# Kernel optimization log

Measured on AMD Instinct MI355X. Metric: run time of the kernel, lower is better.

## Reference

```python
import jax, jax.numpy as jnp
import numpy as np

D_LATENT = 128
WIDTH = 64
MODES = 32
N_LAYERS = 4
N_INST = 8
LIFT_L = 64   # lift_shape = (width, 64)
B = 128
OUT_LEN = 4096
EPS = 1e-5


def _gelu(x):
    return jax.nn.gelu(x, approximate=False)  # torch nn.GELU default = exact erf


def setup_inputs() -> dict:
    key = jax.random.key(0)
    ks = jax.random.split(key, 16)
    n = lambda k, shape, s=0.02: (s * jax.random.normal(k, shape)).astype(jnp.float32)
    spec_scale = 1.0 / (WIDTH * WIDTH)
    return {
        "z": jax.random.normal(ks[0], (B, D_LATENT), dtype=jnp.float32),
        "instrument_params": jax.random.normal(ks[1], (B, N_INST), dtype=jnp.float32),
        "lift_w": n(ks[2], (D_LATENT, WIDTH * LIFT_L)),
        "lift_b": jnp.zeros((WIDTH * LIFT_L,), jnp.float32),
        "inst_w1": n(ks[3], (N_INST, WIDTH), 0.3),
        "inst_b1": jnp.zeros((WIDTH,), jnp.float32),
        "inst_w2": n(ks[4], (WIDTH, WIDTH), 0.1),
        "inst_b2": jnp.zeros((WIDTH,), jnp.float32),
        "spec_w": (spec_scale * jax.random.normal(ks[5], (N_LAYERS, WIDTH, WIDTH, MODES, 2))).astype(jnp.float32),
        "pw_w": n(ks[6], (N_LAYERS, WIDTH, WIDTH), 0.1),   # (layer, out, in)
        "pw_b": jnp.zeros((N_LAYERS, WIDTH), jnp.float32),
        "proj_w1": n(ks[7], (2 * WIDTH, WIDTH), 0.1),      # (out, in)
        "proj_b1": jnp.zeros((2 * WIDTH,), jnp.float32),
        "proj_w2": n(ks[8], (1, 2 * WIDTH), 0.1),
        "proj_b2": jnp.zeros((1,), jnp.float32),
        "out_len": OUT_LEN,
    }


def _interp_linear(x, out_len):
    # torch F.interpolate(mode='linear', align_corners=False)
    in_len = x.shape[-1]
    src = jnp.clip((jnp.arange(out_len, dtype=x.dtype) + 0.5) * (in_len / out_len) - 0.5, 0.0, in_len - 1)
    i0 = jnp.floor(src).astype(jnp.int32)
    i1 = jnp.minimum(i0 + 1, in_len - 1)
    w = src - i0.astype(x.dtype)
    return x[..., i0] * (1.0 - w) + x[..., i1] * w


def _spectral_conv(x, w):
    # x: (B, C, L) real; w: (C_in, C_out, modes, 2)
    L = x.shape[-1]
    xf = jnp.fft.rfft(x, axis=-1)                 # (B, C, L//2+1) complex64
    xr = jnp.real(xf[:, :, :MODES])
    xi = jnp.imag(xf[:, :, :MODES])
    wr, wi = w[..., 0], w[..., 1]
    out_r = jnp.einsum('bim,iom->bom', xr, wr) - jnp.einsum('bim,iom->bom', xi, wi)
    out_i = jnp.einsum('bim,iom->bom', xr, wi) + jnp.einsum('bim,iom->bom', xi, wr)
    n_freq = L // 2 + 1
    of = (out_r + 1j * out_i).astype(xf.dtype)
    of = jnp.pad(of, ((0, 0), (0, 0), (0, n_freq - MODES)))
    return jnp.fft.irfft(of, n=L, axis=-1)


def reference(z, instrument_params, lift_w, lift_b, inst_w1, inst_b1, inst_w2, inst_b2,
              spec_w, pw_w, pw_b, proj_w1, proj_b1, proj_w2, proj_b2, out_len):
    Bz = z.shape[0]
    x = (z @ lift_w + lift_b).reshape(Bz, WIDTH, LIFT_L)
    x = _interp_linear(x, out_len)                              # (B, W, L)
    cond = _gelu(instrument_params @ inst_w1 + inst_b1) @ inst_w2 + inst_b2
    x = x + cond[:, :, None]
    for l in range(N_LAYERS):
        x1 = _spectral_conv(x, spec_w[l])
        x2 = jnp.einsum('bil,oi->bol', x, pw_w[l]) + pw_b[l][None, :, None]
        h = x1 + x2
        mu = h.mean(axis=-1, keepdims=True)
        var = h.var(axis=-1, keepdims=True)                     # biased, like InstanceNorm1d
        x = _gelu((h - mu) * jax.lax.rsqrt(var + EPS))
    h = _gelu(jnp.einsum('bil,oi->bol', x, proj_w1) + proj_b1[None, :, None])
    out = jnp.einsum('bil,oi->bol', h, proj_w2) + proj_b2[None, :, None]
    return out[:, 0, :]                                         # (B, out_len)
```

## Files before the change

kernel.cpp:

```cpp
#include <hip/hip_runtime.h>
#include <math.h>


typedef _Float16 half8 __attribute__((ext_vector_type(8)));
typedef __attribute__((ext_vector_type(4))) float fx4;

__device__ __forceinline__ float gelu_f(float x){
    float u = x*x;
    float a = x * fmaf(-0.1029443f, u, -2.3022083f);
    float e = exp2f(a);
    float r = __builtin_amdgcn_rcpf(1.0f + e);
    return x * r;
}
__device__ __forceinline__ unsigned short f2h(float f){
    union { _Float16 h; unsigned short u; } c;
    c.h = (_Float16)f;
    return c.u;
}
__device__ __forceinline__ float h2f(unsigned short u){
    union { unsigned short u; _Float16 h; } c;
    c.u = u;
    return (float)c.h;
}

static const size_t OFF_XH    = 0;
static const size_t OFF_XT    = 16777216;
static const size_t OFF_TABB  = 33554432;
static const size_t OFF_TABT  = 33685504;
static const size_t OFF_MAH   = 33816576;
static const size_t OFF_PWWH  = 34078720;
static const size_t OFF_W1H   = 34086912;
static const size_t OFF_COND  = 34091008;
static const size_t OFF_STATS = 34099200;
static const size_t OFF_DFTP  = 34115584;
static const size_t OFF_X0    = 38309888;

__global__ void k_tab(unsigned short* __restrict__ tabB, unsigned short* __restrict__ tabT,
                      const float* __restrict__ pww, unsigned short* __restrict__ pwwh,
                      const float* __restrict__ pj1w, unsigned short* __restrict__ w1h){
    int t = blockIdx.x*256 + threadIdx.x;
    if (t < 16384) pwwh[t] = f2h(pww[t]);
    if (t < 8192)  w1h[t]  = f2h(pj1w[t]);
    int m2 = t >> 12, n = t & 4095;
    int m = m2 & 31;
    int r = (m*n) & 4095;
    int r2 = (r >= 2048) ? (r - 4096) : r;
    float a = (float)r2 * 1.5339807878856412e-3f;
    float v = (m2 >= 32) ? sinf(a) : cosf(a);
    tabB[(size_t)m2*4096 + n] = f2h(v);
    tabT[(size_t)n*64 + m2]   = f2h(v * 0.015625f);
}

__global__ __launch_bounds__(64) void k_cond(const float* __restrict__ instp,
        const float* __restrict__ w1, const float* __restrict__ b1,
        const float* __restrict__ w2, const float* __restrict__ b2,
        float* __restrict__ cond){
    int b = blockIdx.x, tid = threadIdx.x;
    __shared__ float ipl[8];
    __shared__ float tl[64];
    if (tid < 8) ipl[tid] = instp[b*8 + tid];
    __syncthreads();
    float s = b1[tid];
    #pragma unroll
    for (int k = 0; k < 8; ++k) s = fmaf(ipl[k], w1[k*64 + tid], s);
    tl[tid] = gelu_f(s);
    __syncthreads();
    float c = b2[tid];
    #pragma unroll 8
    for (int j = 0; j < 64; ++j) c = fmaf(tl[j], w2[j*64 + tid], c);
    cond[b*64 + tid] = c;
}

__global__ __launch_bounds__(256) void k_liftc(const float* __restrict__ z,
        const float* __restrict__ lw, const float* __restrict__ lb,
        const float* __restrict__ cond, float* __restrict__ x0){
    int b = blockIdx.x, q = blockIdx.y;
    int t = threadIdx.x;
    __shared__ float zl[128];
    if (t < 128) zl[t] = z[b*128 + t];
    __syncthreads();
    #pragma unroll
    for (int i = 0; i < 4; ++i){
        int e = q*1024 + i*256 + t;
        float s = lb[e];
        #pragma unroll 8
        for (int d = 0; d < 128; ++d)
            s = fmaf(zl[d], lw[(size_t)d*4096 + e], s);
        x0[(size_t)b*4096 + e] = s + cond[b*64 + (e >> 6)];
    }
}

template<int MODE, int DODFT>
__global__ __launch_bounds__(256) void k_prep(
        const unsigned short* __restrict__ xhp, const float* __restrict__ statsr,
        const unsigned short* __restrict__ tabB, const float* __restrict__ x0,
        unsigned short* __restrict__ xT, float* __restrict__ dftp)
{
    int b = blockIdx.x, ng = blockIdx.y;
    int t = threadIdx.x;
    int w = t >> 6, lane = t & 63;
    int lrow = lane & 15, g = lane >> 4;
    __shared__ __align__(16) unsigned short xl[2][4096];
    __shared__ float xs[(MODE == 2) ? 65*64 : 1];
    int co = t >> 2, nq = t & 3;
    float mu = 0.f, rs = 1.f;
    if (MODE == 1){
        float2 sr = *(const float2*)(statsr + (size_t)(b*64+co)*2);
        mu = sr.x * (1.f/4096.f);
        float var = fmaf(sr.y, 1.f/4096.f, -mu*mu);
        rs = rsqrtf(var + 1e-5f);
    }
    if (MODE == 2){
        const float* xb0 = x0 + (size_t)b*4096;
        #pragma unroll
        for (int i = 0; i < 16; ++i){
            int idx = i*256 + t;
            xs[(idx >> 6)*65 + (idx & 63)] = xb0[idx];
        }
        __syncthreads();
    }
    fx4 acc[4];
    #pragma unroll
    for (int i = 0; i < 4; ++i) acc[i] = (fx4){0.f,0.f,0.f,0.f};

    const unsigned short* hrow = xhp + ((size_t)(b*64+co))*4096 + ng*512 + nq*16;
    unsigned short* xtbase = xT + ((size_t)b*4096 + (size_t)ng*512)*64;

    uint4 cA, cB;
    if (MODE == 1){ cA = *(const uint4*)(hrow); cB = *(const uint4*)(hrow + 8); }
    for (int it = 0; it < 8; ++it){
        int n0 = ng*512 + it*64;
        char* xb = (char*)(&xl[it & 1][0]);
        uint4 nA, nB;
        if (MODE == 1 && it < 7){
            nA = *(const uint4*)(hrow + (it+1)*64);
            nB = *(const uint4*)(hrow + (it+1)*64 + 8);
        }
        unsigned int pk[8];
        if (MODE == 1){
            unsigned int hu[8] = {cA.x,cA.y,cA.z,cA.w,cB.x,cB.y,cB.z,cB.w};
            #pragma unroll
            for (int i = 0; i < 8; ++i){
                float f0 = h2f((unsigned short)(hu[i] & 0xFFFFu));
                float f1 = h2f((unsigned short)(hu[i] >> 16));
                f0 = gelu_f((f0 - mu)*rs);
                f1 = gelu_f((f1 - mu)*rs);
                pk[i] = (unsigned int)f2h(f0) | ((unsigned int)f2h(f1) << 16);
            }
        } else {
            const float* xr = xs + co*65;
            #pragma unroll
            for (int i = 0; i < 8; ++i){
                float v[2];
                #pragma unroll
                for (int q = 0; q < 2; ++q){
                    int n = n0 + nq*16 + i*2 + q;
                    float src = (n + 0.5f)*0.015625f - 0.5f;
                    src = fminf(fmaxf(src, 0.0f), 63.0f);
                    int i0 = (int)src;
                    int i1 = (i0 + 1 > 63) ? 63 : (i0 + 1);
                    float wt = src - (float)i0;
                    v[q] = xr[i0] + wt*(xr[i1] - xr[i0]);
                }
                pk[i] = (unsigned int)f2h(v[0]) | ((unsigned int)f2h(v[1]) << 16);
            }
        }
        unsigned int base = (unsigned int)co*128 + (unsigned int)nq*32;
        unsigned int sw = (unsigned int)((co & 7) << 4);
        *(uint4*)(xb + ((base +  0) ^ sw)) = make_uint4(pk[0],pk[1],pk[2],pk[3]);
        *(uint4*)(xb + ((base + 16) ^ sw)) = make_uint4(pk[4],pk[5],pk[6],pk[7]);
        __syncthreads();

        if (DODFT){
            int m0 = w*16;
            #pragma unroll
            for (int ks = 0; ks < 2; ++ks){
                int kk = ks*32 + g*8;
                half8 af = *(const half8*)(tabB + (size_t)(m0 + lrow)*4096 + n0 + kk);
                #pragma unroll
                for (int ct = 0; ct < 4; ++ct){
                    int row = ct*16 + lrow;
                    unsigned int ba = ((unsigned int)row*128 + (unsigned int)kk*2)
                                      ^ (unsigned int)((row & 7) << 4);
                    half8 bf = *(const half8*)(xb + ba);
                    acc[ct] = __builtin_amdgcn_mfma_f32_16x16x32_f16(af, bf, acc[ct], 0, 0, 0);
                }
            }
        }
        {
            int n = t & 63, coq = t >> 6;
            unsigned int opk[8];
            #pragma unroll
            for (int i = 0; i < 8; ++i){
                int r0 = coq*16 + 2*i, r1 = r0 + 1;
                unsigned int a0 = ((unsigned int)r0*128 + (unsigned int)n*2)
                                  ^ (unsigned int)((r0 & 7) << 4);
                unsigned int a1 = ((unsigned int)r1*128 + (unsigned int)n*2)
                                  ^ (unsigned int)((r1 & 7) << 4);
                unsigned short v0 = *(const unsigned short*)(xb + a0);
                unsigned short v1 = *(const unsigned short*)(xb + a1);
                opk[i] = (unsigned int)v0 | ((unsigned int)v1 << 16);
            }
            unsigned short* dst = xtbase + (size_t)(it*64 + n)*64 + coq*16;
            *(uint4*)dst       = make_uint4(opk[0],opk[1],opk[2],opk[3]);
            *(uint4*)(dst + 8) = make_uint4(opk[4],opk[5],opk[6],opk[7]);
        }
        if (MODE == 1 && it < 7){ cA = nA; cB = nB; }
    }
    if (DODFT){
        int m0 = w*16;
        #pragma unroll
        for (int ct = 0; ct < 4; ++ct){
            float4 v = make_float4(acc[ct][0], acc[ct][1], acc[ct][2], acc[ct][3]);
            *(float4*)(dftp + ((size_t)(b*8+ng)*64 + ct*16 + lrow)*64 + m0 + g*4) = v;
        }
    }
}

__global__ __launch_bounds__(256) void k_mix(const float* __restrict__ dftp,
        const float* __restrict__ specw, unsigned short* __restrict__ mah,
        float* __restrict__ statsr, int l){
    int b = blockIdx.x, coq = blockIdx.y, t = threadIdx.x;
    __shared__ float xm[64*64];
    if (t < 128) statsr[b*128 + t] = 0.f;
    const float* dp = dftp + (size_t)b*8*4096;
    #pragma unroll
    for (int i = 0; i < 4; ++i){
        int e = i*1024 + t*4;
        float4 s = make_float4(0.f,0.f,0.f,0.f);
        #pragma unroll
        for (int ng = 0; ng < 8; ++ng){
            float4 v = *(const float4*)(dp + (size_t)ng*4096 + e);
            s.x += v.x; s.y += v.y; s.z += v.z; s.w += v.w;
        }
        if (e & 32){ s.x = -s.x; s.y = -s.y; s.z = -s.z; s.w = -s.w; }
        *(float4*)(xm + e) = s;
    }
    __syncthreads();
    int mq = t & 3, ciq = (t >> 2) & 3, co_l = t >> 4;
    int co = coq*16 + co_l;
    float yr[8] = {0,0,0,0,0,0,0,0}, yi[8] = {0,0,0,0,0,0,0,0};
    const float* wbase = specw + (size_t)l*262144 + (size_t)co*64 + mq*16;
    #pragma unroll 4
    for (int cil = 0; cil < 16; ++cil){
        int ci = ciq*16 + cil;
        const float* wp = wbase + (size_t)ci*4096;
        float4 w0 = *(const float4*)(wp);
        float4 w1v = *(const float4*)(wp + 4);
        float4 w2v = *(const float4*)(wp + 8);
        float4 w3v = *(const float4*)(wp + 12);
        const float* xc = xm + ci*64 + mq*8;
        float4 r0 = *(const float4*)(xc);
        float4 r1 = *(const float4*)(xc + 4);
        float4 i0 = *(const float4*)(xc + 32);
        float4 i1 = *(const float4*)(xc + 36);
        float wr[8] = {w0.x,w0.z,w1v.x,w1v.z,w2v.x,w2v.z,w3v.x,w3v.z};
        float wi[8] = {w0.y,w0.w,w1v.y,w1v.w,w2v.y,w2v.w,w3v.y,w3v.w};
        float xr[8] = {r0.x,r0.y,r0.z,r0.w,r1.x,r1.y,r1.z,r1.w};
        float xi[8] = {i0.x,i0.y,i0.z,i0.w,i1.x,i1.y,i1.z,i1.w};
        #pragma unroll
        for (int mm = 0; mm < 8; ++mm){
            yr[mm] = fmaf(xr[mm], wr[mm], fmaf(-xi[mm], wi[mm], yr[mm]));
            yi[mm] = fmaf(xr[mm], wi[mm], fmaf( xi[mm], wr[mm], yi[mm]));
        }
    }
    #pragma unroll
    for (int mm = 0; mm < 8; ++mm){
        yr[mm] += __shfl_xor(yr[mm], 4); yr[mm] += __shfl_xor(yr[mm], 8);
        yi[mm] += __shfl_xor(yi[mm], 4); yi[mm] += __shfl_xor(yi[mm], 8);
    }
    if (ciq == 0){
        unsigned short* mb = mah + (size_t)(b*64 + co)*64;
        unsigned int pr[4], pi[4];
        #pragma unroll
        for (int p = 0; p < 4; ++p){
            int m0 = mq*8 + 2*p;
            float s0 = (m0 == 0) ? 0.015625f : 0.03125f;
            pr[p] = (unsigned int)f2h(s0*yr[2*p]) | ((unsigned int)f2h(0.03125f*yr[2*p+1]) << 16);
            pi[p] = (unsigned int)f2h(-0.03125f*yi[2*p]) | ((unsigned int)f2h(-0.03125f*yi[2*p+1]) << 16);
        }
        *(uint4*)(mb + mq*8)      = make_uint4(pr[0],pr[1],pr[2],pr[3]);
        *(uint4*)(mb + 32 + mq*8) = make_uint4(pi[0],pi[1],pi[2],pi[3]);
    }
}

__global__ __launch_bounds__(256, 4) void k_pass3(
        const unsigned short* __restrict__ xT, const unsigned short* __restrict__ tabT,
        const unsigned short* __restrict__ pwwh, const float* __restrict__ pwb,
        const unsigned short* __restrict__ mah, unsigned short* __restrict__ xh,
        float* __restrict__ statsr, int lay)
{
    int b = blockIdx.x, ntg = blockIdx.y;
    int t = threadIdx.x, w = t >> 6, lane = t & 63;
    int lrow = lane & 15, g = lane >> 4;
    int nsl = ntg*256 + w*64;

    half8 A[4][4];
    #pragma unroll
    for (int nt = 0; nt < 4; ++nt){
        int n = nsl + nt*16 + lrow;
        #pragma unroll
        for (int ks = 0; ks < 4; ++ks){
            int k = ks*32 + g*8;
            const unsigned short* src = (k < 64)
                ? (xT   + ((size_t)b*4096 + n)*64 + k)
                : (tabT + (size_t)n*64 + (k - 64));
            A[nt][ks] = *(const half8*)src;
        }
    }
    __shared__ float sred[2][4][64];
    #pragma unroll
    for (int cot = 0; cot < 4; ++cot){
        int co = cot*16 + lrow;
        half8 Bv[4];
        #pragma unroll
        for (int ks = 0; ks < 4; ++ks){
            int k = ks*32 + g*8;
            const unsigned short* src = (k < 64)
                ? (pwwh + ((size_t)lay*64 + co)*64 + k)
                : (mah  + ((size_t)b*64 + co)*64 + (k - 64));
            Bv[ks] = *(const half8*)src;
        }
        fx4 acc[4];
        #pragma unroll
        for (int i = 0; i < 4; ++i) acc[i] = (fx4){0.f,0.f,0.f,0.f};
        #pragma unroll
        for (int ks = 0; ks < 4; ++ks)
            #pragma unroll
            for (int nt = 0; nt < 4; ++nt)
                acc[nt] = __builtin_amdgcn_mfma_f32_16x16x32_f16(A[nt][ks], Bv[ks], acc[nt], 0, 0, 0);

        float pb = pwb[lay*64 + co];
        unsigned short* hr = xh + ((size_t)(b*64+co))*4096;
        float sS = 0.f, sQ = 0.f;
        #pragma unroll
        for (int nt = 0; nt < 4; ++nt){
            float h0 = acc[nt][0] + pb;
            float h1 = acc[nt][1] + pb;
            float h2 = acc[nt][2] + pb;
            float h3 = acc[nt][3] + pb;
            uint2 pk;
            pk.x = (unsigned int)f2h(h0) | ((unsigned int)f2h(h1) << 16);
            pk.y = (unsigned int)f2h(h2) | ((unsigned int)f2h(h3) << 16);
            *(uint2*)(hr + nsl + nt*16 + g*4) = pk;
            sS += (h0 + h1) + (h2 + h3);
            float q = h0*h0;
            q = fmaf(h1, h1, q); q = fmaf(h2, h2, q); q = fmaf(h3, h3, q);
            sQ += q;
        }
        sS += __shfl_xor(sS, 16); sQ += __shfl_xor(sQ, 16);
        sS += __shfl_xor(sS, 32); sQ += __shfl_xor(sQ, 32);
        if (g == 0){
            sred[0][w][cot*16 + lrow] = sS;
            sred[1][w][cot*16 + lrow] = sQ;
        }
    }
    __syncthreads();
    if (t < 64){
        float S = 0.f, Q = 0.f;
        #pragma unroll
        for (int ww = 0; ww < 4; ++ww){ S += sred[0][ww][t]; Q += sred[1][ww][t]; }
        atomicAdd(statsr + (size_t)(b*64+t)*2,     S);
        atomicAdd(statsr + (size_t)(b*64+t)*2 + 1, Q);
    }
}

__global__ __launch_bounds__(512) void k_proj(
        const unsigned short* __restrict__ xT, const unsigned short* __restrict__ w1h,
        const float* __restrict__ b1, const float* __restrict__ w2,
        const float* __restrict__ b2, float* __restrict__ out)
{
    int b = blockIdx.x, ntg = blockIdx.y;
    int t = threadIdx.x, w = t >> 6, lane = t & 63;
    int lrow = lane & 15, g = lane >> 4;
    int o2h = w & 1, nq = w >> 1;
    int nb = ntg*512 + nq*128;

    half8 A[4][2];
    #pragma unroll
    for (int ot = 0; ot < 4; ++ot)
        #pragma unroll
        for (int ks = 0; ks < 2; ++ks)
            A[ot][ks] = *(const half8*)(w1h + (size_t)(o2h*64 + ot*16 + lrow)*64 + ks*32 + g*8);
    float bb[16], wv[16];
    #pragma unroll
    for (int ot = 0; ot < 4; ++ot)
        #pragma unroll
        for (int j = 0; j < 4; ++j){
            int o2 = o2h*64 + ot*16 + g*4 + j;
            bb[ot*4+j] = b1[o2];
            wv[ot*4+j] = w2[o2];
        }
    __shared__ float sred[4][8][2][16];
    for (int tl = 0; tl < 8; ++tl){
        int n = nb + tl*16 + lrow;
        fx4 acc[4];
        #pragma unroll
        for (int i = 0; i < 4; ++i) acc[i] = (fx4){0.f,0.f,0.f,0.f};
        #pragma unroll
        for (int ks = 0; ks < 2; ++ks){
            half8 bf = *(const half8*)(xT + ((size_t)b*4096 + n)*64 + ks*32 + g*8);
            #pragma unroll
            for (int ot = 0; ot < 4; ++ot)
                acc[ot] = __builtin_amdgcn_mfma_f32_16x16x32_f16(A[ot][ks], bf, acc[ot], 0, 0, 0);
        }
        float p = 0.f;
        #pragma unroll
        for (int ot = 0; ot < 4; ++ot)
            #pragma unroll
            for (int j = 0; j < 4; ++j)
                p = fmaf(wv[ot*4+j], gelu_f(acc[ot][j] + bb[ot*4+j]), p);
        p += __shfl_xor(p, 16); p += __shfl_xor(p, 32);
        if (lane < 16) sred[nq][tl][o2h][lane] = p;
    }
    __syncthreads();
    {
        int cl = t & 15, tlf = (t >> 4) & 7, nqf = t >> 7;
        out[(size_t)b*4096 + ntg*512 + t] =
            sred[nqf][tlf][0][cl] + sred[nqf][tlf][1][cl] + b2[0];
    }
}

extern "C" void kernel_launch(void* const* d_in, const int* in_sizes, int n_in,
                              void* d_out, int out_size, void* d_ws, size_t ws_size,
                              hipStream_t stream) {
    (void)in_sizes; (void)n_in; (void)out_size; (void)ws_size;
    const float* z      = (const float*)d_in[0];
    const float* instp  = (const float*)d_in[1];
    const float* lift_w = (const float*)d_in[2];
    const float* lift_b = (const float*)d_in[3];
    const float* iw1    = (const float*)d_in[4];
    const float* ib1    = (const float*)d_in[5];
    const float* iw2    = (const float*)d_in[6];
    const float* ib2    = (const float*)d_in[7];
    const float* specw  = (const float*)d_in[8];
    const float* pww    = (const float*)d_in[9];
    const float* pwb    = (const float*)d_in[10];
    const float* pj1w   = (const float*)d_in[11];
    const float* pj1b   = (const float*)d_in[12];
    const float* pj2w   = (const float*)d_in[13];
    const float* pj2b   = (const float*)d_in[14];

    float* ws = (float*)d_ws;
    unsigned short* xh    = (unsigned short*)(ws + OFF_XH);
    unsigned short* xT    = (unsigned short*)(ws + OFF_XT);
    unsigned short* tabB  = (unsigned short*)(ws + OFF_TABB);
    unsigned short* tabT  = (unsigned short*)(ws + OFF_TABT);
    unsigned short* mah   = (unsigned short*)(ws + OFF_MAH);
    unsigned short* pwwh  = (unsigned short*)(ws + OFF_PWWH);
    unsigned short* w1h   = (unsigned short*)(ws + OFF_W1H);
    float* cond   = ws + OFF_COND;
    float* statsr = ws + OFF_STATS;
    float* dftp   = ws + OFF_DFTP;
    float* x0     = ws + OFF_X0;
    float* out    = (float*)d_out;

    k_tab  <<<dim3(1024),  dim3(256), 0, stream>>>(tabB, tabT, pww, pwwh, pj1w, w1h);
    k_cond <<<dim3(128),   dim3(64),  0, stream>>>(instp, iw1, ib1, iw2, ib2, cond);
    k_liftc<<<dim3(128,4), dim3(256), 0, stream>>>(z, lift_w, lift_b, cond, x0);

    for (int l = 0; l < 4; ++l){
        if (l == 0)
            k_prep<2,1><<<dim3(128,8), dim3(256), 0, stream>>>(xh, statsr, tabB, x0, xT, dftp);
        else
            k_prep<1,1><<<dim3(128,8), dim3(256), 0, stream>>>(xh, statsr, tabB, x0, xT, dftp);
        k_mix  <<<dim3(128,4),  dim3(256), 0, stream>>>(dftp, specw, mah, statsr, l);
        k_pass3<<<dim3(128,16), dim3(256), 0, stream>>>(xT, tabT, pwwh, pwb, mah, xh, statsr, l);
    }
    k_prep<1,0><<<dim3(128,8), dim3(256), 0, stream>>>(xh, statsr, tabB, x0, xT, dftp);
    k_proj    <<<dim3(128,8),  dim3(512), 0, stream>>>(xT, w1h, pj1b, pj2w, pj2b, out);
}
```

Baseline: 456.5 us.

## Fuse final instance-norm/GELU prep into projection kernel via swizzled LDS transpose

Removes the last k_prep launch and folds its work into the projection kernel. The new k_proj2 reads the raw fp16 layer output, applies instance norm from the stats buffer and GELU, and transposes the result through XOR-swizzled shared memory, with the next chunk's global load software-pipelined. This drops one kernel launch and the write and re-read of the transposed xT buffer. In exchange it adds per-element LDS gathers for the MFMA operands and a barrier in every iteration, and the block shrinks to 256 threads.

```diff
diff --git a/kernel.cpp b/kernel.cpp
--- a/kernel.cpp
+++ b/kernel.cpp
@@ -365,16 +365,25 @@
     }
 }
 
-__global__ __launch_bounds__(512) void k_proj(
-        const unsigned short* __restrict__ xT, const unsigned short* __restrict__ w1h,
-        const float* __restrict__ b1, const float* __restrict__ w2,
-        const float* __restrict__ b2, float* __restrict__ out)
+__global__ __launch_bounds__(256) void k_proj2(
+        const unsigned short* __restrict__ xhp, const float* __restrict__ statsr,
+        const unsigned short* __restrict__ w1h, const float* __restrict__ b1,
+        const float* __restrict__ w2, const float* __restrict__ b2,
+        float* __restrict__ out)
 {
-    int b = blockIdx.x, ntg = blockIdx.y;
+    int b = blockIdx.x, ng = blockIdx.y;
     int t = threadIdx.x, w = t >> 6, lane = t & 63;
     int lrow = lane & 15, g = lane >> 4;
-    int o2h = w & 1, nq = w >> 1;
-    int nb = ntg*512 + nq*128;
+    int o2h = w & 1, nhalf = w >> 1;
+    __shared__ __align__(16) unsigned short xl[2][4096];
+    __shared__ float sred[2][2][2][2][16];
+
+    int ci = t >> 2, nq = t & 3;
+    float2 sr = *(const float2*)(statsr + (size_t)(b*64+ci)*2);
+    float mu = sr.x * (1.f/4096.f);
+    float var = fmaf(sr.y, 1.f/4096.f, -mu*mu);
+    float rs = rsqrtf(var + 1e-5f);
+    const unsigned short* hrow = xhp + ((size_t)(b*64+ci))*4096 + ng*512 + nq*16;
 
     half8 A[4][2];
     #pragma unroll
@@ -391,33 +400,81 @@
             bb[ot*4+j] = b1[o2];
             wv[ot*4+j] = w2[o2];
         }
-    __shared__ float sred[4][8][2][16];
-    for (int tl = 0; tl < 8; ++tl){
-        int n = nb + tl*16 + lrow;
-        fx4 acc[4];
-        #pragma unroll
-        for (int i = 0; i < 4; ++i) acc[i] = (fx4){0.f,0.f,0.f,0.f};
-        #pragma unroll
-        for (int ks = 0; ks < 2; ++ks){
-            half8 bf = *(const half8*)(xT + ((size_t)b*4096 + n)*64 + ks*32 + g*8);
+    float bias2 = b2[0];
+
+    uint4 cA = *(const uint4*)(hrow);
+    uint4 cB = *(const uint4*)(hrow + 8);
+    for (int it = 0; it < 8; ++it){
+        char* xb = (char*)(&xl[it & 1][0]);
+        uint4 nA, nB;
+        if (it < 7){
+            nA = *(const uint4*)(hrow + (it+1)*64);
+            nB = *(const uint4*)(hrow + (it+1)*64 + 8);
+        }
+        unsigned int pk[8];
+        {
+            unsigned int hu[8] = {cA.x,cA.y,cA.z,cA.w,cB.x,cB.y,cB.z,cB.w};
+            #pragma unroll
+            for (int i = 0; i < 8; ++i){
+                float f0 = h2f((unsigned short)(hu[i] & 0xFFFFu));
+                float f1 = h2f((unsigned short)(hu[i] >> 16));
+                f0 = gelu_f((f0 - mu)*rs);
+                f1 = gelu_f((f1 - mu)*rs);
+                pk[i] = (unsigned int)f2h(f0) | ((unsigned int)f2h(f1) << 16);
+            }
+        }
+        unsigned int base = (unsigned int)ci*128 + (unsigned int)nq*32;
+        unsigned int sw = (unsigned int)((ci & 7) << 4);
+        *(uint4*)(xb + ((base +  0) ^ sw)) = make_uint4(pk[0],pk[1],pk[2],pk[3]);
+        *(uint4*)(xb + ((base + 16) ^ sw)) = make_uint4(pk[4],pk[5],pk[6],pk[7]);
+        __syncthreads();
+
+        if (it > 0 && t < 64){
+            int nh = t >> 5, rem = t & 31, ntf = rem >> 4, cl = rem & 15;
+            out[(size_t)b*4096 + ng*512 + (it-1)*64 + t] =
+                sred[(it-1)&1][nh][ntf][0][cl] + sred[(it-1)&1][nh][ntf][1][cl] + bias2;
+        }
+
+        #pragma unroll
+        for (int nt = 0; nt < 2; ++nt){
+            int n_l = nhalf*32 + nt*16 + lrow;
+            half8 Bf[2];
+            #pragma unroll
+            for (int ks = 0; ks < 2; ++ks){
+                union { unsigned short u[8]; half8 v; } bu;
+                #pragma unroll
+                for (int e = 0; e < 8; ++e){
+                    int cie = ks*32 + g*8 + e;
+                    unsigned int ba = ((unsigned int)cie*128 + (unsigned int)n_l*2)
+                                      ^ (unsigned int)((cie & 7) << 4);
+                    bu.u[e] = *(const unsigned short*)(xb + ba);
+                }
+                Bf[ks] = bu.v;
+            }
+            fx4 acc[4];
+            #pragma unroll
+            for (int i = 0; i < 4; ++i) acc[i] = (fx4){0.f,0.f,0.f,0.f};
+            #pragma unroll
+            for (int ks = 0; ks < 2; ++ks)
+                #pragma unroll
+                for (int ot = 0; ot < 4; ++ot)
+                    acc[ot] = __builtin_amdgcn_mfma_f32_16x16x32_f16(A[ot][ks], Bf[ks], acc[ot], 0, 0, 0);
+            float p = 0.f;
             #pragma unroll
             for (int ot = 0; ot < 4; ++ot)
-                acc[ot] = __builtin_amdgcn_mfma_f32_16x16x32_f16(A[ot][ks], bf, acc[ot], 0, 0, 0);
-        }
-        float p = 0.f;
-        #pragma unroll
-        for (int ot = 0; ot < 4; ++ot)
-            #pragma unroll
-            for (int j = 0; j < 4; ++j)
-                p = fmaf(wv[ot*4+j], gelu_f(acc[ot][j] + bb[ot*4+j]), p);
-        p += __shfl_xor(p, 16); p += __shfl_xor(p, 32);
-        if (lane < 16) sred[nq][tl][o2h][lane] = p;
+                #pragma unroll
+                for (int j = 0; j < 4; ++j)
+                    p = fmaf(wv[ot*4+j], gelu_f(acc[ot][j] + bb[ot*4+j]), p);
+            p += __shfl_xor(p, 16); p += __shfl_xor(p, 32);
+            if (lane < 16) sred[it & 1][nhalf][nt][o2h][lane] = p;
+        }
+        if (it < 7){ cA = nA; cB = nB; }
     }
     __syncthreads();
-    {
-        int cl = t & 15, tlf = (t >> 4) & 7, nqf = t >> 7;
-        out[(size_t)b*4096 + ntg*512 + t] =
-            sred[nqf][tlf][0][cl] + sred[nqf][tlf][1][cl] + b2[0];
+    if (t < 64){
+        int nh = t >> 5, rem = t & 31, ntf = rem >> 4, cl = rem & 15;
+        out[(size_t)b*4096 + ng*512 + 7*64 + t] =
+            sred[1][nh][ntf][0][cl] + sred[1][nh][ntf][1][cl] + bias2;
     }
 }
 
@@ -467,6 +524,5 @@
         k_mix  <<<dim3(128,4),  dim3(256), 0, stream>>>(dftp, specw, mah, statsr, l);
         k_pass3<<<dim3(128,16), dim3(256), 0, stream>>>(xT, tabT, pwwh, pwb, mah, xh, statsr, l);
     }
-    k_prep<1,0><<<dim3(128,8), dim3(256), 0, stream>>>(xh, statsr, tabB, x0, xT, dftp);
-    k_proj    <<<dim3(128,8),  dim3(512), 0, stream>>>(xT, w1h, pj1b, pj2w, pj2b, out);
-}
+    k_proj2<<<dim3(128,8), dim3(256), 0, stream>>>(xh, statsr, w1h, pj1b, pj2w, pj2b, out);
+}
```

After: 442.3 us. -3.1%, faster.
